# Performance work log

Hardware: AMD Instinct MI355X
Metric: run time of the kernel (lower is better)

Reference implementation:

```python
import jax, jax.numpy as jnp
import numpy as np

N = 768          # number of nodes (points)
F = 128          # n_invariant_feat_hidden (0e channels)
V = 64           # n_vectors_hidden (1e channels)
S_RO, V_RO = 128, 64   # readout_mlp_irreps widths
S_OUT, V_OUT = 64, 32  # output_irreps widths
R_HID = 16       # radial MLP hidden width
AVG = 64.0       # avg_num_neighbors normalization
N_LAYERS = 2     # num_interactions


def _w(key, shape):
    fan_in = shape[-2] if len(shape) > 1 else 1
    return jax.random.normal(key, shape, jnp.float32) / np.sqrt(fan_in)


def setup_inputs() -> dict:
    key = jax.random.key(0)
    ks = jax.random.split(key, 16)
    x = jax.random.normal(ks[0], (N, 3), jnp.float32) * 2.0
    idx = np.arange(N)
    s, r = np.meshgrid(idx, idx, indexing='ij')
    mask = s != r  # fully connected graph, no self edges
    senders = jnp.asarray(s[mask], jnp.int32)
    receivers = jnp.asarray(r[mask], jnp.int32)
    return {
        'x': x,
        'senders': senders,
        'receivers': receivers,
        'embed': _w(ks[1], (1, F)),            # species embedding (num_species=1)
        'Wr1': _w(ks[2], (N_LAYERS, 1, R_HID)),
        'Wr2s': _w(ks[3], (N_LAYERS, R_HID, F)),
        'Wr2v': _w(ks[4], (N_LAYERS, R_HID, V)),
        'Wsv': _w(ks[5], (N_LAYERS, F, V)),
        'Wss': _w(ks[6], (N_LAYERS, F, F)),
        'Wvs': _w(ks[7], (N_LAYERS, V, F)),
        'Wvv': _w(ks[8], (N_LAYERS, V, V)),
        'Wro_s1': _w(ks[9], (F, S_RO)),
        'Wro_s2': _w(ks[10], (S_RO, S_OUT)),
        'Wro_v1': _w(ks[11], (V, V_RO)),
        'Wro_v2': _w(ks[12], (V_RO, V_OUT)),
    }


def reference(x, senders, receivers, embed, Wr1, Wr2s, Wr2v, Wsv, Wss, Wvs, Wvv,
              Wro_s1, Wro_s2, Wro_v1, Wro_v2):
    n = x.shape[0]
    vec = x[senders] - x[receivers]                 # [E, 3] pairwise displacement
    d = jnp.linalg.norm(vec, axis=-1, keepdims=True)  # [E, 1] radial basis (identity)
    sh1 = vec / (d + 1e-8)                          # l=1 spherical harmonics (unit vector)

    hs = jnp.broadcast_to(embed[0], (n, F))         # node_specie == 0 for all nodes
    hv = jnp.zeros((n, V, 3), x.dtype)

    for l in range(N_LAYERS):
        rf = jax.nn.silu(d @ Wr1[l])                # [E, R_HID] radial MLP
        ws = rf @ Wr2s[l]                           # [E, F] scalar path radial weights
        wv = rf @ Wr2v[l]                           # [E, V] vector path radial weights
        hs_e = hs[senders]                          # gather sender scalars [E, F]
        m_s = hs_e * ws                             # 0e x 0e -> 0e messages
        m_v = ((hs_e @ Wsv[l]) * wv)[:, :, None] * sh1[:, None, :]  # 0e x 1e -> 1e [E,V,3]
        agg_s = jax.ops.segment_sum(m_s, receivers, num_segments=n) / AVG
        agg_v = jax.ops.segment_sum(m_v, receivers, num_segments=n) / AVG
        inv = jnp.sum(agg_v * agg_v, axis=-1)       # 1e (x) 1e -> 0e contraction [N, V]
        hs = jax.nn.silu(hs + agg_s @ Wss[l] + inv @ Wvs[l])
        hv = hv + jnp.einsum('nvd,vw->nwd', agg_v, Wvv[l])

    ro_s = jax.nn.silu(hs @ Wro_s1) @ Wro_s2        # [N, S_OUT]
    ro_v = jnp.einsum('nvd,vw->nwd',
                      jnp.einsum('nvd,vw->nwd', hv, Wro_v1), Wro_v2)  # [N, V_OUT, 3]
    return jnp.concatenate([ro_s, ro_v.reshape(n, -1)], axis=-1)       # [N, S_OUT + 3*V_OUT]
```

## Files before the change

### kernel.cpp

```cpp
#include <hip/hip_runtime.h>
#include <hip/hip_bf16.h>
#include <math.h>

#define NN 768
#define FF 128
#define VV 64
#define RH 16
#define SPLITK 24
#define SEND_PER_KC 32
#define NITER 4
#define KSTEPS 384
#define NT_S 8
#define NT_V 16
#define MB_N 24

typedef __attribute__((ext_vector_type(8))) short bf16x8_t;
typedef __attribute__((ext_vector_type(4))) float f32x4;

__device__ __forceinline__ float silu_f(float a) {
  return a * __builtin_amdgcn_rcpf(1.0f + __expf(-a));
}

__device__ __forceinline__ short f2bf(float f) {
  __hip_bfloat16 h = __float2bfloat16(f);
  return __builtin_bit_cast(short, h);
}

__device__ __forceinline__ float bf2f(unsigned short v) {
  return __builtin_bit_cast(float, (unsigned)v << 16);
}

__global__ __launch_bounds__(256) void layer0_kernel(
    const float* __restrict__ x,
    const float* __restrict__ Wr1,
    const float* __restrict__ Wr2s,
    const float* __restrict__ Wr2v,
    const float* __restrict__ embed,
    const float* __restrict__ Wsv0,
    const float* __restrict__ Wss,
    const float* __restrict__ Wvs,
    const float* __restrict__ Wvv,
    const float* __restrict__ Wsv1,
    float* __restrict__ hs,
    float* __restrict__ hv,
    unsigned short* __restrict__ Bs,
    unsigned short* __restrict__ Bv)
{
  __shared__ float accT[256 * 33];
  __shared__ float red8[8][32];
  __shared__ float fin[64];
  __shared__ float cvs[64];
  __shared__ float as_l[FF];
  __shared__ float av_l[192];
  __shared__ float inv_l[VV];
  __shared__ float hsn[FF];
  __shared__ float hsv_l[VV];
  __shared__ float redn[256];

  const int r   = blockIdx.x;
  const int tid = threadIdx.x;

  if (tid < 64) {
    float a = 0.f;
    #pragma unroll 8
    for (int f = 0; f < FF; ++f) a += embed[f] * Wsv0[f * VV + tid];
    cvs[tid] = a;
  }

  float wr1[RH];
  #pragma unroll
  for (int hh = 0; hh < RH; ++hh) wr1[hh] = Wr1[hh];

  const float xr0 = x[r * 3 + 0], xr1 = x[r * 3 + 1], xr2 = x[r * 3 + 2];

  float acc[64];
  #pragma unroll
  for (int i = 0; i < 64; ++i) acc[i] = 0.f;

  #pragma unroll
  for (int ss = 0; ss < 3; ++ss) {
    const int s = tid + ss * 256;
    const float vx = x[s * 3 + 0] - xr0;
    const float vy = x[s * 3 + 1] - xr1;
    const float vz = x[s * 3 + 2] - xr2;
    const float d  = __builtin_amdgcn_sqrtf(vx * vx + vy * vy + vz * vz);
    const float iv = __builtin_amdgcn_rcpf(d + 1e-8f);
    const float ux = vx * iv, uy = vy * iv, uz = vz * iv;
    #pragma unroll
    for (int h = 0; h < RH; ++h) {
      const float rf = silu_f(d * wr1[h]);
      acc[h * 4 + 0] += rf;
      acc[h * 4 + 1] += rf * ux;
      acc[h * 4 + 2] += rf * uy;
      acc[h * 4 + 3] += rf * uz;
    }
  }

  {
    #pragma unroll
    for (int i = 0; i < 32; ++i) accT[tid * 33 + i] = acc[i];
    __syncthreads();
    {
      const int j2 = tid & 31, q2 = tid >> 5;
      float a0 = 0.f, a1 = 0.f;
      #pragma unroll 8
      for (int rr = 0; rr < 32; rr += 2) {
        a0 += accT[(q2 * 32 + rr) * 33 + j2];
        a1 += accT[(q2 * 32 + rr + 1) * 33 + j2];
      }
      red8[q2][j2] = a0 + a1;
    }
    __syncthreads();
    if (tid < 32) {
      float a = 0.f;
      #pragma unroll
      for (int g = 0; g < 8; ++g) a += red8[g][tid];
      fin[tid] = a;
    }
    __syncthreads();

    #pragma unroll
    for (int i = 0; i < 32; ++i) accT[tid * 33 + i] = acc[32 + i];
    __syncthreads();
    {
      const int j2 = tid & 31, q2 = tid >> 5;
      float a0 = 0.f, a1 = 0.f;
      #pragma unroll 8
      for (int rr = 0; rr < 32; rr += 2) {
        a0 += accT[(q2 * 32 + rr) * 33 + j2];
        a1 += accT[(q2 * 32 + rr + 1) * 33 + j2];
      }
      red8[q2][j2] = a0 + a1;
    }
    __syncthreads();
    if (tid < 32) {
      float a = 0.f;
      #pragma unroll
      for (int g = 0; g < 8; ++g) a += red8[g][tid];
      fin[32 + tid] = a;
    }
    __syncthreads();
  }

  if (tid < FF) {
    float a = 0.f;
    #pragma unroll
    for (int hh = 0; hh < RH; ++hh) a += fin[hh * 4] * Wr2s[hh * FF + tid];
    as_l[tid] = a * embed[tid] * (1.0f / 64.0f);
  }
  if (tid < 192) {
    const int v = tid / 3, d = tid - v * 3;
    float a = 0.f;
    #pragma unroll
    for (int hh = 0; hh < RH; ++hh) a += fin[hh * 4 + 1 + d] * Wr2v[hh * VV + v];
    av_l[tid] = a * cvs[v] * (1.0f / 64.0f);
  }
  __syncthreads();

  if (tid < VV) {
    const float a0 = av_l[tid * 3 + 0], a1 = av_l[tid * 3 + 1], a2 = av_l[tid * 3 + 2];
    inv_l[tid] = a0 * a0 + a1 * a1 + a2 * a2;
  }
  __syncthreads();

  {
    const int f = tid & 127, part = tid >> 7;
    float a = 0.f;
    const float* wp = Wss + (part * 64) * FF + f;
    #pragma unroll 8
    for (int kk = 0; kk < 64; ++kk) a += as_l[part * 64 + kk] * wp[kk * FF];
    const float* vp = Wvs + (part * 32) * FF + f;
    #pragma unroll 8
    for (int vv = 0; vv < 32; ++vv) a += inv_l[part * 32 + vv] * vp[vv * FF];
    redn[part * 128 + f] = a;
  }
  __syncthreads();

  if (tid < FF) {
    const float hnew = silu_f(embed[tid] + redn[tid] + redn[128 + tid]);
    hs[(size_t)r * FF + tid] = hnew;
    hsn[tid] = hnew;
  }
  if (tid < 192) {
    const int w = tid / 3, d = tid - w * 3;
    float a = 0.f;
    #pragma unroll 8
    for (int v = 0; v < VV; ++v) a += av_l[v * 3 + d] * Wvv[v * VV + w];
    hv[(size_t)r * 192 + tid] = a;
  }
  __syncthreads();

  {
    const int v = tid & 63, part = tid >> 6;
    float a = 0.f;
    const float* wp = Wsv1 + (part * 32) * VV + v;
    #pragma unroll 8
    for (int f = 0; f < 32; ++f) a += hsn[part * 32 + f] * wp[f * VV];
    redn[tid] = a;
  }
  __syncthreads();
  if (tid < VV)
    hsv_l[tid] = redn[tid] + redn[64 + tid] + redn[128 + tid] + redn[192 + tid];
  __syncthreads();

  {
    const float* W2s = Wr2s + RH * FF;
    const float* W2v = Wr2v + RH * VV;
    const int s     = r;
    const int kstep = s >> 1;
    const int lbase = (s & 1) << 5;
    const float xs0 = x[s * 3 + 0], xs1 = x[s * 3 + 1], xs2 = x[s * 3 + 2];

    #pragma unroll
    for (int k = 0; k < 3; ++k) {
      const int item  = tid + k * 256;
      const int ntile = item >> 5;
      const int li    = item & 31;
      const int lane  = lbase + li;
      const int hb    = ((li >> 4) & 1) * 8;

      bf16x8_t o;
      if (ntile < NT_S) {
        const int f = ntile * 16 + (li & 15);
        const float hf = hsn[f] * 0.015625f;
        #pragma unroll
        for (int e = 0; e < 8; ++e)
          o[e] = f2bf(hf * W2s[(hb + e) * FF + f]);
        *(bf16x8_t*)&Bs[((size_t)(kstep * NT_S + ntile) * 64 + lane) * 8] = o;
      } else {
        const int nt2 = ntile - NT_S;
        const int n   = nt2 * 16 + (li & 15);
        int v; float scale;
        if (n < 192) {
          const int dd = n >> 6; v = n & 63;
          const float xd = (dd == 0) ? xs0 : ((dd == 1) ? xs1 : xs2);
          scale = xd * hsv_l[v] * 0.015625f;
        } else {
          v = n - 192; scale = hsv_l[v] * 0.015625f;
        }
        #pragma unroll
        for (int e = 0; e < 8; ++e)
          o[e] = f2bf(scale * W2v[(hb + e) * VV + v]);
        *(bf16x8_t*)&Bv[((size_t)(kstep * NT_V + nt2) * 64 + lane) * 8] = o;
      }
    }
  }
}

__global__ __launch_bounds__(256) void edge_gemm(
    const float* __restrict__ x,
    const unsigned short* __restrict__ Bs,
    const unsigned short* __restrict__ Bv,
    const float* __restrict__ Wr1,
    unsigned short* __restrict__ Ps,
    unsigned short* __restrict__ Pv)
{
  __shared__ unsigned short A_lds[4 * 2 * 64 * 8];
  __shared__ unsigned short G_lds[4 * 2 * 64 * 8];

  const int wg = ((blockIdx.x & 7) * 72) + (blockIdx.x >> 3);
  const int kc = wg / MB_N;
  const int mb = wg - kc * MB_N;

  const int tid  = threadIdx.x;
  const int lane = tid & 63;
  const int w    = tid >> 6;

  float wr1[RH];
  #pragma unroll
  for (int h = 0; h < RH; ++h) wr1[h] = Wr1[h];

  const int r_local = tid & 31;
  const int s_ii    = tid >> 5;
  const int r = mb * 32 + r_local;
  const int mt_w  = r_local >> 4;
  const int ks_w  = s_ii >> 1;
  const int lane0 = (r_local & 15) + ((s_ii & 1) << 5);

  const float xr0 = x[r * 3 + 0], xr1 = x[r * 3 + 1], xr2 = x[r * 3 + 2];
  float sx[NITER], sy[NITER], sz[NITER];
  #pragma unroll
  for (int it = 0; it < NITER; ++it) {
    const int s = kc * SEND_PER_KC + it * 8 + s_ii;
    sx[it] = x[s * 3 + 0]; sy[it] = x[s * 3 + 1]; sz[it] = x[s * 3 + 2];
  }

  f32x4 accS[4], accV[8];
  #pragma unroll
  for (int i = 0; i < 4; ++i) accS[i] = (f32x4){0.f, 0.f, 0.f, 0.f};
  #pragma unroll
  for (int i = 0; i < 8; ++i) accV[i] = (f32x4){0.f, 0.f, 0.f, 0.f};

  for (int it = 0; it < NITER; ++it) {
    {
      const float vx = sx[it] - xr0;
      const float vy = sy[it] - xr1;
      const float vz = sz[it] - xr2;
      const float dd = __builtin_amdgcn_sqrtf(vx * vx + vy * vy + vz * vz);
      const float iv = __builtin_amdgcn_rcpf(dd + 1e-8f);
      float sv[RH];
      #pragma unroll
      for (int h = 0; h < RH; ++h) sv[h] = silu_f(dd * wr1[h]);
      bf16x8_t o0, o1, g0, g1;
      #pragma unroll
      for (int h = 0; h < 8; ++h) {
        o0[h] = f2bf(sv[h]);
        o1[h] = f2bf(sv[h + 8]);
        g0[h] = f2bf(sv[h] * iv);
        g1[h] = f2bf(sv[h + 8] * iv);
      }
      const int off0 = ((ks_w * 2 + mt_w) * 64 + lane0) * 8;
      *(bf16x8_t*)&A_lds[off0]       = o0;
      *(bf16x8_t*)&A_lds[off0 + 128] = o1;
      *(bf16x8_t*)&G_lds[off0]       = g0;
      *(bf16x8_t*)&G_lds[off0 + 128] = g1;
    }
    __syncthreads();

    const int kgb = kc * (SEND_PER_KC / 2) + it * 4;
    #pragma unroll
    for (int ks = 0; ks < 4; ++ks) {
      const bf16x8_t b0 =
          *(const bf16x8_t*)&Bs[((size_t)((kgb + ks) * NT_S + 2 * w) * 64 + lane) * 8];
      const bf16x8_t b1 =
          *(const bf16x8_t*)&Bs[((size_t)((kgb + ks) * NT_S + 2 * w + 1) * 64 + lane) * 8];
      bf16x8_t bv[4];
      #pragma unroll
      for (int j = 0; j < 4; ++j)
        bv[j] = *(const bf16x8_t*)&Bv[((size_t)((kgb + ks) * NT_V + 4 * w + j) * 64 + lane) * 8];
      #pragma unroll
      for (int mt = 0; mt < 2; ++mt) {
        const int aoff = ((ks * 2 + mt) * 64 + lane) * 8;
        const bf16x8_t a  = *(const bf16x8_t*)&A_lds[aoff];
        const bf16x8_t ag = *(const bf16x8_t*)&G_lds[aoff];
        accS[mt * 2 + 0] = __builtin_amdgcn_mfma_f32_16x16x32_bf16(a, b0, accS[mt * 2 + 0], 0, 0, 0);
        accS[mt * 2 + 1] = __builtin_amdgcn_mfma_f32_16x16x32_bf16(a, b1, accS[mt * 2 + 1], 0, 0, 0);
        #pragma unroll
        for (int j = 0; j < 4; ++j)
          accV[mt * 4 + j] = __builtin_amdgcn_mfma_f32_16x16x32_bf16(ag, bv[j], accV[mt * 4 + j], 0, 0, 0);
      }
    }
    __syncthreads();
  }

  const int rowq = (lane >> 4) << 2;
  #pragma unroll
  for (int j = 0; j < 2; ++j) {
    const int col = (2 * w + j) * 16 + (lane & 15);
    #pragma unroll
    for (int mt = 0; mt < 2; ++mt) {
      #pragma unroll
      for (int reg = 0; reg < 4; ++reg) {
        const int row = mb * 32 + mt * 16 + rowq + reg;
        Ps[((size_t)kc * NN + row) * FF + col] =
            (unsigned short)f2bf(accS[mt * 2 + j][reg]);
      }
    }
  }
  #pragma unroll
  for (int j = 0; j < 4; ++j) {
    const int col = (4 * w + j) * 16 + (lane & 15);
    #pragma unroll
    for (int mt = 0; mt < 2; ++mt) {
      #pragma unroll
      for (int reg = 0; reg < 4; ++reg) {
        const int row = mb * 32 + mt * 16 + rowq + reg;
        Pv[((size_t)kc * NN + row) * 256 + col] =
            (unsigned short)f2bf(accV[mt * 4 + j][reg]);
      }
    }
  }
}

__global__ __launch_bounds__(512) void final_kernel(
    const unsigned short* __restrict__ Ps,
    const unsigned short* __restrict__ Pv,
    const float* __restrict__ x,
    const float* __restrict__ hs,
    const float* __restrict__ hv,
    const float* __restrict__ Wss,
    const float* __restrict__ Wvs,
    const float* __restrict__ Wvv,
    const float* __restrict__ Wro_s1,
    const float* __restrict__ Wro_s2,
    const float* __restrict__ Wro_v1,
    const float* __restrict__ Wro_v2,
    float* __restrict__ out)
{
  __shared__ float as_l[FF];
  __shared__ float pvs_l[256];
  __shared__ float av_l[192];
  __shared__ float inv_l[VV];
  __shared__ float hsn[FF];
  __shared__ float hv_l[192];
  __shared__ float red[512];
  __shared__ float red2[384];
  __shared__ float t1[FF];
  __shared__ float tv1[192];
  const int n = blockIdx.x, t = threadIdx.x;

  if (t < FF) {
    float a = 0.f;
    #pragma unroll
    for (int kc = 0; kc < SPLITK; ++kc)
      a += bf2f(Ps[((size_t)kc * NN + n) * FF + t]);
    as_l[t] = a;
  } else if (t < 384) {
    const int cc = t - 128;
    float a = 0.f;
    #pragma unroll
    for (int kc = 0; kc < SPLITK; ++kc)
      a += bf2f(Pv[((size_t)kc * NN + n) * 256 + cc]);
    pvs_l[cc] = a;
  }
  __syncthreads();

  if (t < VV) {
    const float base = pvs_l[192 + t];
    const float a0 = pvs_l[t]       - x[n * 3 + 0] * base;
    const float a1 = pvs_l[64 + t]  - x[n * 3 + 1] * base;
    const float a2 = pvs_l[128 + t] - x[n * 3 + 2] * base;
    av_l[t * 3 + 0] = a0; av_l[t * 3 + 1] = a1; av_l[t * 3 + 2] = a2;
    inv_l[t] = a0 * a0 + a1 * a1 + a2 * a2;
  }
  __syncthreads();

  {
    const int f = t & 127, part = t >> 7;
    float acc = 0.f;
    const float* wp = Wss + (part * 32) * FF + f;
    #pragma unroll 8
    for (int kk = 0; kk < 32; ++kk) acc += as_l[part * 32 + kk] * wp[kk * FF];
    const float* vp = Wvs + (part * 16) * FF + f;
    #pragma unroll 8
    for (int vv = 0; vv < 16; ++vv) acc += inv_l[part * 16 + vv] * vp[vv * FF];
    red[part * 128 + f] = acc;
  }
  __syncthreads();

  if (t < FF) {
    hsn[t] = silu_f(hs[n * FF + t] + red[t] + red[128 + t] + red[256 + t] + red[384 + t]);
  }
  if (t < 384) {
    const int part = t / 192, j = t - part * 192;
    const int wv = j / 3, d = j - wv * 3;
    float acc = 0.f;
    const float* vp = Wvv + (part * 32) * VV + wv;
    #pragma unroll 8
    for (int v = 0; v < 32; ++v) acc += av_l[(part * 32 + v) * 3 + d] * vp[v * VV];
    red2[part * 192 + j] = acc;
  }
  __syncthreads();

  if (t < 192) hv_l[t] = hv[n * 192 + t] + red2[t] + red2[192 + t];
  __syncthreads();

  {
    const int f = t & 127, part = t >> 7;
    float acc = 0.f;
    const float* wp = Wro_s1 + (part * 32) * FF + f;
    #pragma unroll 8
    for (int kk = 0; kk < 32; ++kk) acc += hsn[part * 32 + kk] * wp[kk * FF];
    red[part * 128 + f] = acc;
  }
  __syncthreads();
  if (t < FF) t1[t] = silu_f(red[t] + red[128 + t] + red[256 + t] + red[384 + t]);
  if (t < 384) {
    const int part = t / 192, j = t - part * 192;
    const int wv = j / 3, d = j - wv * 3;
    float acc = 0.f;
    const float* vp = Wro_v1 + (part * 32) * VV + wv;
    #pragma unroll 8
    for (int v = 0; v < 32; ++v) acc += hv_l[(part * 32 + v) * 3 + d] * vp[v * VV];
    red2[part * 192 + j] = acc;
  }
  __syncthreads();
  if (t < 192) tv1[t] = red2[t] + red2[192 + t];
  if (t < 256) {
    const int o = t & 63, part = t >> 6;
    float acc = 0.f;
    const float* wp = Wro_s2 + (part * 32) * 64 + o;
    #pragma unroll 8
    for (int f = 0; f < 32; ++f) acc += t1[part * 32 + f] * wp[f * 64];
    red[t] = acc;
  }
  __syncthreads();
  if (t < 64) out[n * 160 + t] = red[t] + red[64 + t] + red[128 + t] + red[192 + t];
  if (t < 192) {
    const int part = t / 96, j = t - part * 96;
    const int w2 = j / 3, d = j - w2 * 3;
    float acc = 0.f;
    const float* vp = Wro_v2 + (part * 32) * 32 + w2;
    #pragma unroll 8
    for (int wv = 0; wv < 32; ++wv) acc += tv1[(part * 32 + wv) * 3 + d] * vp[wv * 32];
    red2[part * 96 + j] = acc;
  }
  __syncthreads();
  if (t < 96) out[n * 160 + 64 + t] = red2[t] + red2[96 + t];
}

extern "C" void kernel_launch(void* const* d_in, const int* in_sizes, int n_in,
                              void* d_out, int out_size, void* d_ws, size_t ws_size,
                              hipStream_t stream) {
  const float* x      = (const float*)d_in[0];
  const float* embed  = (const float*)d_in[3];
  const float* Wr1    = (const float*)d_in[4];
  const float* Wr2s   = (const float*)d_in[5];
  const float* Wr2v   = (const float*)d_in[6];
  const float* Wsv    = (const float*)d_in[7];
  const float* Wss    = (const float*)d_in[8];
  const float* Wvs    = (const float*)d_in[9];
  const float* Wvv    = (const float*)d_in[10];
  const float* Wro_s1 = (const float*)d_in[11];
  const float* Wro_s2 = (const float*)d_in[12];
  const float* Wro_v1 = (const float*)d_in[13];
  const float* Wro_v2 = (const float*)d_in[14];

  float* ws_f = (float*)d_ws;
  float* hs    = ws_f;
  float* hv    = hs + NN * FF;
  unsigned short* Ps = (unsigned short*)(hv + NN * 192);
  unsigned short* Pv = Ps + (size_t)SPLITK * NN * FF;
  unsigned short* Bs = Pv + (size_t)SPLITK * NN * 256;
  unsigned short* Bv = Bs + (size_t)12288 * 128;
  float* out = (float*)d_out;

  layer0_kernel<<<NN, 256, 0, stream>>>(
      x, Wr1, Wr2s, Wr2v, embed, Wsv, Wss, Wvs, Wvv, Wsv + FF * VV,
      hs, hv, Bs, Bv);

  edge_gemm<<<MB_N * SPLITK, 256, 0, stream>>>(
      x, Bs, Bv, Wr1 + RH, Ps, Pv);
  final_kernel<<<NN, 512, 0, stream>>>(
      Ps, Pv, x, hs, hv, Wss + FF * FF, Wvs + VV * FF, Wvv + VV * VV,
      Wro_s1, Wro_s2, Wro_v1, Wro_v2, out);
}
```

Before: 54.44 us.

## Batch four nodes per block in final kernel and retune edge GEMM split-K

The final kernel now handles four nodes per workgroup, so each weight load from global memory feeds four accumulators instead of one, and the launch uses a quarter as many blocks. Some split reductions become single-thread full-length loops. Separately, the edge GEMM split-K factor rises from 24 to 32 with fewer senders per chunk, which gives more workgroups but more partial buffers for the final kernel to sum. The larger split means more bf16 partial traffic, and fewer final blocks may lower parallelism.

After: 64.39 us. 18.3% more time.

```diff
diff --git a/kernel.cpp b/kernel.cpp
--- a/kernel.cpp
+++ b/kernel.cpp
@@ -6,9 +6,9 @@
 #define FF 128
 #define VV 64
 #define RH 16
-#define SPLITK 24
-#define SEND_PER_KC 32
-#define NITER 4
+#define SPLITK 32
+#define SEND_PER_KC 24
+#define NITER 3
 #define KSTEPS 384
 #define NT_S 8
 #define NT_V 16
@@ -258,7 +258,7 @@
   __shared__ unsigned short A_lds[4 * 2 * 64 * 8];
   __shared__ unsigned short G_lds[4 * 2 * 64 * 8];
 
-  const int wg = ((blockIdx.x & 7) * 72) + (blockIdx.x >> 3);
+  const int wg = ((blockIdx.x & 7) * 96) + (blockIdx.x >> 3);
   const int kc = wg / MB_N;
   const int mb = wg - kc * MB_N;
 
@@ -387,116 +387,161 @@
     const float* __restrict__ Wro_v2,
     float* __restrict__ out)
 {
-  __shared__ float as_l[FF];
-  __shared__ float pvs_l[256];
-  __shared__ float av_l[192];
-  __shared__ float inv_l[VV];
-  __shared__ float hsn[FF];
-  __shared__ float hv_l[192];
-  __shared__ float red[512];
-  __shared__ float red2[384];
-  __shared__ float t1[FF];
-  __shared__ float tv1[192];
-  const int n = blockIdx.x, t = threadIdx.x;
-
-  if (t < FF) {
+  __shared__ float as_l[4][FF];
+  __shared__ float pvs_l[4][256];
+  __shared__ float av_l[4][192];
+  __shared__ float inv_l[4][VV];
+  __shared__ float hsn[4][FF];
+  __shared__ float hv_l[4][192];
+  __shared__ float red[4][512];
+  __shared__ float t1[4][FF];
+  __shared__ float tv1[4][192];
+  const int n0 = blockIdx.x * 4;
+  const int t  = threadIdx.x;
+
+  {
+    const int g = t >> 7, c = t & 127;
     float a = 0.f;
     #pragma unroll
     for (int kc = 0; kc < SPLITK; ++kc)
-      a += bf2f(Ps[((size_t)kc * NN + n) * FF + t]);
-    as_l[t] = a;
-  } else if (t < 384) {
-    const int cc = t - 128;
+      a += bf2f(Ps[((size_t)kc * NN + n0 + g) * FF + c]);
+    as_l[g][c] = a;
+  }
+  #pragma unroll
+  for (int i = 0; i < 2; ++i) {
+    const int item = t + i * 512;
+    const int g = item >> 8, c = item & 255;
     float a = 0.f;
     #pragma unroll
     for (int kc = 0; kc < SPLITK; ++kc)
-      a += bf2f(Pv[((size_t)kc * NN + n) * 256 + cc]);
-    pvs_l[cc] = a;
-  }
-  __syncthreads();
-
-  if (t < VV) {
-    const float base = pvs_l[192 + t];
-    const float a0 = pvs_l[t]       - x[n * 3 + 0] * base;
-    const float a1 = pvs_l[64 + t]  - x[n * 3 + 1] * base;
-    const float a2 = pvs_l[128 + t] - x[n * 3 + 2] * base;
-    av_l[t * 3 + 0] = a0; av_l[t * 3 + 1] = a1; av_l[t * 3 + 2] = a2;
-    inv_l[t] = a0 * a0 + a1 * a1 + a2 * a2;
+      a += bf2f(Pv[((size_t)kc * NN + n0 + g) * 256 + c]);
+    pvs_l[g][c] = a;
+  }
+  __syncthreads();
+
+  if (t < 256) {
+    const int g = t >> 6, v = t & 63;
+    const float base = pvs_l[g][192 + v];
+    const float a0 = pvs_l[g][v]       - x[(n0 + g) * 3 + 0] * base;
+    const float a1 = pvs_l[g][64 + v]  - x[(n0 + g) * 3 + 1] * base;
+    const float a2 = pvs_l[g][128 + v] - x[(n0 + g) * 3 + 2] * base;
+    av_l[g][v * 3 + 0] = a0; av_l[g][v * 3 + 1] = a1; av_l[g][v * 3 + 2] = a2;
+    inv_l[g][v] = a0 * a0 + a1 * a1 + a2 * a2;
   }
   __syncthreads();
 
   {
     const int f = t & 127, part = t >> 7;
-    float acc = 0.f;
+    float a0 = 0.f, a1 = 0.f, a2 = 0.f, a3 = 0.f;
     const float* wp = Wss + (part * 32) * FF + f;
-    #pragma unroll 8
-    for (int kk = 0; kk < 32; ++kk) acc += as_l[part * 32 + kk] * wp[kk * FF];
+    #pragma unroll 4
+    for (int kk = 0; kk < 32; ++kk) {
+      const float w = wp[kk * FF];
+      const int k = part * 32 + kk;
+      a0 += as_l[0][k] * w; a1 += as_l[1][k] * w;
+      a2 += as_l[2][k] * w; a3 += as_l[3][k] * w;
+    }
     const float* vp = Wvs + (part * 16) * FF + f;
-    #pragma unroll 8
-    for (int vv = 0; vv < 16; ++vv) acc += inv_l[part * 16 + vv] * vp[vv * FF];
-    red[part * 128 + f] = acc;
-  }
-  __syncthreads();
-
-  if (t < FF) {
-    hsn[t] = silu_f(hs[n * FF + t] + red[t] + red[128 + t] + red[256 + t] + red[384 + t]);
-  }
-  if (t < 384) {
-    const int part = t / 192, j = t - part * 192;
-    const int wv = j / 3, d = j - wv * 3;
-    float acc = 0.f;
-    const float* vp = Wvv + (part * 32) * VV + wv;
-    #pragma unroll 8
-    for (int v = 0; v < 32; ++v) acc += av_l[(part * 32 + v) * 3 + d] * vp[v * VV];
-    red2[part * 192 + j] = acc;
-  }
-  __syncthreads();
-
-  if (t < 192) hv_l[t] = hv[n * 192 + t] + red2[t] + red2[192 + t];
+    #pragma unroll 4
+    for (int vv = 0; vv < 16; ++vv) {
+      const float w = vp[vv * FF];
+      const int k = part * 16 + vv;
+      a0 += inv_l[0][k] * w; a1 += inv_l[1][k] * w;
+      a2 += inv_l[2][k] * w; a3 += inv_l[3][k] * w;
+    }
+    const int o = part * 128 + f;
+    red[0][o] = a0; red[1][o] = a1; red[2][o] = a2; red[3][o] = a3;
+  }
+  __syncthreads();
+
+  {
+    const int g = t >> 7, f = t & 127;
+    hsn[g][f] = silu_f(hs[(size_t)(n0 + g) * FF + f] +
+                       red[g][f] + red[g][128 + f] + red[g][256 + f] + red[g][384 + f]);
+  }
+  if (t < 192) {
+    const int w = t / 3, d = t - w * 3;
+    float a0 = 0.f, a1 = 0.f, a2 = 0.f, a3 = 0.f;
+    #pragma unroll 4
+    for (int v = 0; v < VV; ++v) {
+      const float wv_ = Wvv[v * VV + w];
+      a0 += av_l[0][v * 3 + d] * wv_; a1 += av_l[1][v * 3 + d] * wv_;
+      a2 += av_l[2][v * 3 + d] * wv_; a3 += av_l[3][v * 3 + d] * wv_;
+    }
+    hv_l[0][t] = hv[(size_t)(n0 + 0) * 192 + t] + a0;
+    hv_l[1][t] = hv[(size_t)(n0 + 1) * 192 + t] + a1;
+    hv_l[2][t] = hv[(size_t)(n0 + 2) * 192 + t] + a2;
+    hv_l[3][t] = hv[(size_t)(n0 + 3) * 192 + t] + a3;
+  }
   __syncthreads();
 
   {
     const int f = t & 127, part = t >> 7;
-    float acc = 0.f;
+    float a0 = 0.f, a1 = 0.f, a2 = 0.f, a3 = 0.f;
     const float* wp = Wro_s1 + (part * 32) * FF + f;
-    #pragma unroll 8
-    for (int kk = 0; kk < 32; ++kk) acc += hsn[part * 32 + kk] * wp[kk * FF];
-    red[part * 128 + f] = acc;
-  }
-  __syncthreads();
-  if (t < FF) t1[t] = silu_f(red[t] + red[128 + t] + red[256 + t] + red[384 + t]);
-  if (t < 384) {
-    const int part = t / 192, j = t - part * 192;
-    const int wv = j / 3, d = j - wv * 3;
-    float acc = 0.f;
-    const float* vp = Wro_v1 + (part * 32) * VV + wv;
-    #pragma unroll 8
-    for (int v = 0; v < 32; ++v) acc += hv_l[(part * 32 + v) * 3 + d] * vp[v * VV];
-    red2[part * 192 + j] = acc;
-  }
-  __syncthreads();
-  if (t < 192) tv1[t] = red2[t] + red2[192 + t];
+    #pragma unroll 4
+    for (int kk = 0; kk < 32; ++kk) {
+      const float w = wp[kk * FF];
+      const int k = part * 32 + kk;
+      a0 += hsn[0][k] * w; a1 += hsn[1][k] * w;
+      a2 += hsn[2][k] * w; a3 += hsn[3][k] * w;
+    }
+    const int o = part * 128 + f;
+    red[0][o] = a0; red[1][o] = a1; red[2][o] = a2; red[3][o] = a3;
+  }
+  __syncthreads();
+  {
+    const int g = t >> 7, f = t & 127;
+    t1[g][f] = silu_f(red[g][f] + red[g][128 + f] + red[g][256 + f] + red[g][384 + f]);
+  }
+  if (t < 192) {
+    const int w = t / 3, d = t - w * 3;
+    float a0 = 0.f, a1 = 0.f, a2 = 0.f, a3 = 0.f;
+    #pragma unroll 4
+    for (int v = 0; v < VV; ++v) {
+      const float wv_ = Wro_v1[v * VV + w];
+      a0 += hv_l[0][v * 3 + d] * wv_; a1 += hv_l[1][v * 3 + d] * wv_;
+      a2 += hv_l[2][v * 3 + d] * wv_; a3 += hv_l[3][v * 3 + d] * wv_;
+    }
+    tv1[0][t] = a0; tv1[1][t] = a1; tv1[2][t] = a2; tv1[3][t] = a3;
+  }
+  __syncthreads();
+
   if (t < 256) {
     const int o = t & 63, part = t >> 6;
-    float acc = 0.f;
+    float a0 = 0.f, a1 = 0.f, a2 = 0.f, a3 = 0.f;
     const float* wp = Wro_s2 + (part * 32) * 64 + o;
-    #pragma unroll 8
-    for (int f = 0; f < 32; ++f) acc += t1[part * 32 + f] * wp[f * 64];
-    red[t] = acc;
-  }
-  __syncthreads();
-  if (t < 64) out[n * 160 + t] = red[t] + red[64 + t] + red[128 + t] + red[192 + t];
-  if (t < 192) {
-    const int part = t / 96, j = t - part * 96;
+    #pragma unroll 4
+    for (int f2 = 0; f2 < 32; ++f2) {
+      const float w = wp[f2 * 64];
+      const int k = part * 32 + f2;
+      a0 += t1[0][k] * w; a1 += t1[1][k] * w;
+      a2 += t1[2][k] * w; a3 += t1[3][k] * w;
+    }
+    const int oo = part * 64 + o;
+    red[0][oo] = a0; red[1][oo] = a1; red[2][oo] = a2; red[3][oo] = a3;
+  }
+  if (t >= 256 && t < 352) {
+    const int j = t - 256;
     const int w2 = j / 3, d = j - w2 * 3;
-    float acc = 0.f;
-    const float* vp = Wro_v2 + (part * 32) * 32 + w2;
-    #pragma unroll 8
-    for (int wv = 0; wv < 32; ++wv) acc += tv1[(part * 32 + wv) * 3 + d] * vp[wv * 32];
-    red2[part * 96 + j] = acc;
-  }
-  __syncthreads();
-  if (t < 96) out[n * 160 + 64 + t] = red2[t] + red2[96 + t];
+    float a0 = 0.f, a1 = 0.f, a2 = 0.f, a3 = 0.f;
+    #pragma unroll 4
+    for (int wv = 0; wv < VV; ++wv) {
+      const float w = Wro_v2[wv * 32 + w2];
+      a0 += tv1[0][wv * 3 + d] * w; a1 += tv1[1][wv * 3 + d] * w;
+      a2 += tv1[2][wv * 3 + d] * w; a3 += tv1[3][wv * 3 + d] * w;
+    }
+    out[(size_t)(n0 + 0) * 160 + 64 + j] = a0;
+    out[(size_t)(n0 + 1) * 160 + 64 + j] = a1;
+    out[(size_t)(n0 + 2) * 160 + 64 + j] = a2;
+    out[(size_t)(n0 + 3) * 160 + 64 + j] = a3;
+  }
+  __syncthreads();
+  if (t < 256) {
+    const int g = t >> 6, o = t & 63;
+    out[(size_t)(n0 + g) * 160 + o] =
+        red[g][o] + red[g][64 + o] + red[g][128 + o] + red[g][192 + o];
+  }
 }
 
 extern "C" void kernel_launch(void* const* d_in, const int* in_sizes, int n_in,
@@ -531,7 +576,7 @@
 
   edge_gemm<<<MB_N * SPLITK, 256, 0, stream>>>(
       x, Bs, Bv, Wr1 + RH, Ps, Pv);
-  final_kernel<<<NN, 512, 0, stream>>>(
+  final_kernel<<<NN / 4, 512, 0, stream>>>(
       Ps, Pv, x, hs, hv, Wss + FF * FF, Wvs + VV * FF, Wvv + VV * VV,
       Wro_s1, Wro_s2, Wro_v1, Wro_v2, out);
 }
```
